# Performance work log

Measured on AMD Instinct MI355X. Metric: run time of the kernel, lower is better.

## Reference

```python
import jax, jax.numpy as jnp
import numpy as np

D_MODEL = 256   # c / input_dim
D_INNER = 512   # expand * d_model
D_STATE = 16
DT_RANK = 16    # ceil(d_model / 16)
D_CONV = 3


def setup_inputs() -> dict:
    key = jax.random.key(0)
    ks = jax.random.split(key, 8)
    s = lambda k, shape, sc=0.02: (jax.random.normal(k, shape, jnp.float32) * sc)
    feature = jax.random.normal(ks[0], (16, D_MODEL, 32, 32), jnp.float32)
    A_init = jnp.broadcast_to(jnp.arange(1, D_STATE + 1, dtype=jnp.float32), (D_INNER, D_STATE))
    return {
        "feature": feature,
        "norm_w": jnp.ones((D_MODEL,), jnp.float32),                 # RMSNorm weight
        "w_in": s(ks[1], (D_MODEL, 2 * D_INNER)),                     # in_proj (no bias)
        "conv_w": s(ks[2], (D_INNER, D_CONV), 0.1),                   # depthwise conv kernel
        "conv_b": jnp.zeros((D_INNER,), jnp.float32),                 # conv bias
        "w_xproj": s(ks[3], (D_INNER, DT_RANK + 2 * D_STATE)),        # x_proj (no bias)
        "w_dt": s(ks[4], (DT_RANK, D_INNER)),                         # dt_proj weight
        "b_dt": s(ks[5], (D_INNER,), 0.1),                            # dt_proj bias
        "A_log": jnp.log(A_init),                                     # [d_inner, d_state]
        "D": jnp.ones((D_INNER,), jnp.float32),                       # skip param
        "w_out": s(ks[6], (D_INNER, D_MODEL)),                        # out_proj (no bias)
    }


def _mamba_residual(x, norm_w, w_in, conv_w, conv_b, w_xproj, w_dt, b_dt, A_log, D, w_out):
    # x: [B, L, d_model] where B = h*w (spatial positions) and L = original batch b
    B, L, _ = x.shape
    # RMSNorm
    xn = x * jax.lax.rsqrt(jnp.mean(x * x, axis=-1, keepdims=True) + 1e-5) * norm_w
    # input projection -> [B, L, 2*d_inner]
    xr = xn @ w_in
    xm, res = jnp.split(xr, 2, axis=-1)
    # depthwise causal conv1d along L
    xc = jnp.transpose(xm, (0, 2, 1))                 # [B, d_inner, L]
    k = conv_w[:, None, :]                             # [d_inner, 1, d_conv]
    xc = jax.lax.conv_general_dilated(
        xc, k, window_strides=(1,), padding=[(D_CONV - 1, 0)],
        feature_group_count=D_INNER)
    xc = xc + conv_b[None, :, None]
    xm = jax.nn.silu(jnp.transpose(xc, (0, 2, 1)))    # [B, L, d_inner]
    # selective SSM
    A = -jnp.exp(A_log)                                # [d_inner, d_state]
    dbc = xm @ w_xproj                                 # [B, L, dt_rank + 2*d_state]
    delta, Bm, Cm = jnp.split(dbc, [DT_RANK, DT_RANK + D_STATE], axis=-1)
    delta = jax.nn.softplus(delta @ w_dt + b_dt)       # [B, L, d_inner]
    dA = jnp.exp(delta[..., None] * A)                 # [B, L, d_inner, d_state]
    dBu = delta[..., None] * Bm[:, :, None, :] * xm[..., None]

    def step(h, inp):
        dA_t, dBu_t, C_t = inp                         # [B,d,n], [B,d,n], [B,n]
        h = dA_t * h + dBu_t
        y = jnp.einsum('bdn,bn->bd', h, C_t)
        return h, y

    h0 = jnp.zeros((B, D_INNER, D_STATE), xm.dtype)
    _, ys = jax.lax.scan(
        step, h0,
        (dA.transpose(1, 0, 2, 3), dBu.transpose(1, 0, 2, 3), Cm.transpose(1, 0, 2)))
    y = ys.transpose(1, 0, 2) + xm * D                 # [B, L, d_inner]
    y = y * jax.nn.silu(res)
    return y @ w_out + x                               # residual add


def reference(feature, norm_w, w_in, conv_w, conv_b, w_xproj, w_dt, b_dt, A_log, D, w_out):
    b, c, h, w = feature.shape
    # [b,c,h,w] -> [h*w, b, c]: Mamba batch = spatial positions, seq = samples
    x = feature.transpose(0, 2, 3, 1).reshape(b, h * w, c).transpose(1, 0, 2)
    out = _mamba_residual(x, norm_w, w_in, conv_w, conv_b, w_xproj, w_dt, b_dt, A_log, D, w_out)
    out = out.transpose(1, 0, 2).reshape(b, h, w, c).transpose(0, 3, 1, 2)
    return out
```

## Files before the change

### kernel.cpp

```cpp
#include <hip/hip_runtime.h>
#include <hip/hip_bf16.h>
#include <math.h>

#define NPOS   1024
#define NSAMP  16
#define DMODEL 256
#define DINNER 512
#define DSTATE 16
#define DTRANK 16
#define MROWS  (NPOS*NSAMP)
#define LOG2E  1.44269504f

typedef __attribute__((ext_vector_type(8))) short short8;
typedef __attribute__((ext_vector_type(4))) float f32x4;

__device__ __forceinline__ unsigned short f2bf(float f) {
    unsigned int u = __builtin_bit_cast(unsigned int, f);
    u = u + 0x7FFFu + ((u >> 16) & 1u);
    return (unsigned short)(u >> 16);
}
__device__ __forceinline__ float bf2f(short b) {
    unsigned int u = ((unsigned int)(unsigned short)b) << 16;
    return __builtin_bit_cast(float, u);
}
__device__ __forceinline__ float fsilu(float x) {
    return x * __builtin_amdgcn_rcpf(1.f + __expf(-x));
}
__device__ __forceinline__ void gl16(const void* g, void* l) {
    __builtin_amdgcn_global_load_lds((const __attribute__((address_space(1))) void*)g,
                                     (__attribute__((address_space(3))) void*)l, 16, 0, 0);
}

__global__ __launch_bounds__(256) void kprep(const float* __restrict__ w_in,
                                             const float* __restrict__ w_out,
                                             const float* __restrict__ w_xproj,
                                             unsigned short* __restrict__ w_inT,
                                             unsigned short* __restrict__ w_outT,
                                             unsigned short* __restrict__ wxT) {
    int idx = blockIdx.x * 256 + threadIdx.x;
    if (idx < 262144) {
        int n = idx >> 8, k = idx & 255;
        w_inT[idx] = f2bf(w_in[(size_t)k * 1024 + n]);
    } else if (idx < 262144 + 131072) {
        int i = idx - 262144;
        int c = i >> 9, k = i & 511;
        w_outT[i] = f2bf(w_out[(size_t)k * DMODEL + c]);
    } else {
        int i = idx - 262144 - 131072;
        int j = i >> 9, k = i & 511;
        wxT[i] = f2bf(w_xproj[(size_t)k * 48 + j]);
    }
}

__global__ __launch_bounds__(256) void knorm(const float* __restrict__ feat,
                                             const float* __restrict__ norm_w,
                                             unsigned short* __restrict__ xnT) {
    __shared__ float part[4][64];
    __shared__ float ssc[64];
    __shared__ char tile[64 * 520];
    int t = threadIdx.x;
    int s = blockIdx.x, p0 = blockIdx.y * 64;
    int pl = t & 63, cg = t >> 6;
    const float* base = feat + (size_t)s * (DMODEL * NPOS) + p0 + pl;
    float vals[64];
    float ss = 0.f;
    #pragma unroll
    for (int j = 0; j < 64; ++j) {
        float v = base[(size_t)(cg * 64 + j) * NPOS];
        vals[j] = v;
        ss += v * v;
    }
    part[cg][pl] = ss;
    __syncthreads();
    if (t < 64) {
        float tot = part[0][t] + part[1][t] + part[2][t] + part[3][t];
        ssc[t] = rsqrtf(tot * (1.f / DMODEL) + 1e-5f);
    }
    __syncthreads();
    float sc = ssc[pl];
    unsigned short* trow = (unsigned short*)(tile + pl * 520);
    #pragma unroll
    for (int j = 0; j < 64; ++j)
        trow[cg * 64 + j] = f2bf(vals[j] * sc * norm_w[cg * 64 + j]);
    __syncthreads();
    int p = t >> 2, cb = (t & 3) * 64;
    const unsigned short* srow = (const unsigned short*)(tile + p * 520);
    unsigned short* orow = xnT + (size_t)((s << 10) + p0 + p) * DMODEL + cb;
    #pragma unroll
    for (int j8 = 0; j8 < 8; ++j8) {
        short8 v;
        #pragma unroll
        for (int jj = 0; jj < 8; ++jj) v[jj] = srow[cb + j8 * 8 + jj];
        *reinterpret_cast<short8*>(orow + j8 * 8) = v;
    }
}

__global__ __launch_bounds__(256) void k1_mfma(const unsigned short* __restrict__ xnT,
                                               const unsigned short* __restrict__ w_inT,
                                               unsigned short* __restrict__ xmbf,
                                               unsigned short* __restrict__ gbf) {
    __shared__ char As[128 * 128];
    __shared__ char Bs[128 * 128];
    int t = threadIdx.x;
    int m0 = blockIdx.y * 128, n0 = blockIdx.x * 128;
    int l = t & 63, w = t >> 6;
    int wm = w & 1, wn = w >> 1, g = l >> 4, lr = l & 15;

    f32x4 acc[4][4] = {};
    for (int k0 = 0; k0 < DMODEL; k0 += 64) {
        if (k0) __syncthreads();
        #pragma unroll
        for (int q = 0; q < 4; ++q) {
            int chunk = q * 256 + t;
            int row = chunk >> 3, cb = chunk & 7;
            gl16(xnT  + (size_t)(m0 + row) * DMODEL + k0 + cb * 8, As + chunk * 16);
            gl16(w_inT + (size_t)(n0 + row) * DMODEL + k0 + cb * 8, Bs + chunk * 16);
        }
        __syncthreads();
        #pragma unroll
        for (int ks = 0; ks < 2; ++ks) {
            short8 a[4], b[4];
            #pragma unroll
            for (int mi = 0; mi < 4; ++mi)
                a[mi] = *reinterpret_cast<short8*>(As + (wm * 64 + mi * 16 + lr) * 128 + ks * 64 + g * 16);
            #pragma unroll
            for (int ni = 0; ni < 4; ++ni)
                b[ni] = *reinterpret_cast<short8*>(Bs + (wn * 64 + ni * 16 + lr) * 128 + ks * 64 + g * 16);
            #pragma unroll
            for (int mi = 0; mi < 4; ++mi)
                #pragma unroll
                for (int ni = 0; ni < 4; ++ni)
                    acc[mi][ni] = __builtin_amdgcn_mfma_f32_16x16x32_bf16(a[mi], b[ni], acc[mi][ni], 0, 0, 0);
        }
    }
    bool isRes = (n0 >= 512);
    #pragma unroll
    for (int mi = 0; mi < 4; ++mi) {
        #pragma unroll
        for (int r = 0; r < 4; ++r) {
            int m = m0 + wm * 64 + mi * 16 + g * 4 + r;
            #pragma unroll
            for (int ni = 0; ni < 4; ++ni) {
                int n = n0 + wn * 64 + ni * 16 + lr;
                float v = acc[mi][ni][r];
                if (isRes) gbf[(size_t)m * DINNER + n - 512] = f2bf(fsilu(v));
                else       xmbf[(size_t)m * DINNER + n] = f2bf(v);
            }
        }
    }
}

__global__ __launch_bounds__(256) void k3_mfma(const unsigned short* __restrict__ xmbf,
                                               const float* __restrict__ conv_w,
                                               const float* __restrict__ conv_b,
                                               const unsigned short* __restrict__ wxT,
                                               float* __restrict__ dbc) {
    __shared__ char Ws[48 * 64];
    __shared__ char Xs[64 * 64];
    int t = threadIdx.x;
    int m0 = blockIdx.x * 64;
    int s = m0 >> 10;
    int l = t & 63, w = t >> 6, g = l >> 4, lr = l & 15;
    int xrow = t >> 2, xck = t & 3;
    int m = m0 + xrow;
    f32x4 acc[3] = {};
    for (int k0 = 0; k0 < DINNER; k0 += 32) {
        if (k0) __syncthreads();
        if (t < 192) {
            int j = t >> 2, ck = t & 3;
            *reinterpret_cast<short8*>(Ws + j * 64 + ck * 16) =
                *reinterpret_cast<const short8*>(wxT + (size_t)j * DINNER + k0 + ck * 8);
        }
        {
            int d0 = k0 + xck * 8;
            const unsigned short* r0 = xmbf + (size_t)m * DINNER + d0;
            short8 x0 = *reinterpret_cast<const short8*>(r0);
            short8 x1 = {}, x2 = {};
            if (s >= 1) x1 = *reinterpret_cast<const short8*>(r0 - 1024 * DINNER);
            if (s >= 2) x2 = *reinterpret_cast<const short8*>(r0 - 2048 * DINNER);
            short8 v;
            #pragma unroll
            for (int j = 0; j < 8; ++j) {
                int dd = d0 + j;
                float cv = conv_b[dd] + conv_w[dd * 3 + 2] * bf2f(x0[j])
                         + conv_w[dd * 3 + 1] * bf2f(x1[j]) + conv_w[dd * 3 + 0] * bf2f(x2[j]);
                v[j] = (short)f2bf(fsilu(cv));
            }
            *reinterpret_cast<short8*>(Xs + xrow * 64 + xck * 16) = v;
        }
        __syncthreads();
        short8 b = *reinterpret_cast<short8*>(Xs + (w * 16 + lr) * 64 + g * 16);
        #pragma unroll
        for (int aj = 0; aj < 3; ++aj) {
            short8 a = *reinterpret_cast<short8*>(Ws + (aj * 16 + lr) * 64 + g * 16);
            acc[aj] = __builtin_amdgcn_mfma_f32_16x16x32_bf16(a, b, acc[aj], 0, 0, 0);
        }
    }
    int mc = m0 + w * 16 + lr;
    #pragma unroll
    for (int aj = 0; aj < 3; ++aj)
        *reinterpret_cast<f32x4*>(dbc + (size_t)mc * 48 + aj * 16 + g * 4) = acc[aj];
}

__global__ __launch_bounds__(256) void k5_scan(const unsigned short* __restrict__ xmbf,
                                               const unsigned short* __restrict__ gbf,
                                               const float* __restrict__ dbc,
                                               const float* __restrict__ w_dt,
                                               const float* __restrict__ b_dt,
                                               const float* __restrict__ A_log,
                                               const float* __restrict__ Dp,
                                               const float* __restrict__ conv_w,
                                               const float* __restrict__ conv_b,
                                               unsigned short* __restrict__ ybf) {
    int p = blockIdx.x >> 1;
    int d = ((blockIdx.x & 1) << 8) + threadIdx.x;
    float wdt[DTRANK];
    #pragma unroll
    for (int r = 0; r < DTRANK; ++r) wdt[r] = w_dt[r * DINNER + d];
    float Ar0 = -__expf(A_log[d * DSTATE]);
    bool geo = true;
    #pragma unroll
    for (int n = 1; n < DSTATE; ++n) {
        float An = -__expf(A_log[d * DSTATE + n]);
        geo = geo && (fabsf(An - (n + 1) * Ar0) <= 1e-4f * (n + 1));
    }
    float c0 = LOG2E * Ar0;
    float w0 = conv_w[d * 3 + 0], w1 = conv_w[d * 3 + 1], w2 = conv_w[d * 3 + 2];
    float cb = conv_b[d], Dv = Dp[d], bdt = b_dt[d];
    float h[DSTATE];
    #pragma unroll
    for (int n = 0; n < DSTATE; ++n) h[n] = 0.f;
    float x1 = 0.f, x2 = 0.f;

    for (int s = 0; s < NSAMP; ++s) {
        int m = (s << 10) + p;
        size_t off = (size_t)m * DINNER + d;
        float xc = bf2f((short)xmbf[off]);
        float gv = bf2f((short)gbf[off]);
        float cv = cb + w2 * xc + w1 * x1 + w0 * x2;
        x2 = x1; x1 = xc;
        float u = fsilu(cv);
        const float* row = dbc + (size_t)m * 48;
        float dp = bdt;
        #pragma unroll
        for (int r = 0; r < DTRANK; ++r) dp += row[r] * wdt[r];
        float delta = (dp > 20.f) ? dp : __logf(1.f + __expf(dp));
        float du = delta * u;
        float yv = 0.f;
        if (geo) {
            float rg = exp2f(delta * c0);
            float rr = rg;
            #pragma unroll
            for (int n = 0; n < DSTATE; ++n) {
                h[n] = rr * h[n] + du * row[16 + n];
                yv += h[n] * row[32 + n];
                rr *= rg;
            }
        } else {
            #pragma unroll
            for (int n = 0; n < DSTATE; ++n) {
                float An = -__expf(A_log[d * DSTATE + n]);
                float dA = __expf(delta * An);
                h[n] = dA * h[n] + du * row[16 + n];
                yv += h[n] * row[32 + n];
            }
        }
        ybf[off] = f2bf((yv + u * Dv) * gv);
    }
}

__global__ __launch_bounds__(256) void k6_mfma(const unsigned short* __restrict__ ybf,
                                               const unsigned short* __restrict__ w_outT,
                                               const float* __restrict__ feat,
                                               float* __restrict__ out) {
    __shared__ char lds[2 * 128 * 80];
    char* Ws = lds;
    char* Ys = lds + 128 * 80;
    int t = threadIdx.x;
    int m0 = blockIdx.x * 128;
    int cblk = blockIdx.y * 128;
    int s = m0 >> 10, p0 = m0 & 1023;
    int i = t & 127, c0 = t >> 7;
    int l = t & 63, w = t >> 6;
    int wm = w & 1, wn = w >> 1, g = l >> 4, lr = l & 15;

    f32x4 acc[4][4] = {};
    for (int k0 = 0; k0 < DINNER; k0 += 32) {
        if (k0) __syncthreads();
        #pragma unroll
        for (int cc = 0; cc < 2; ++cc) {
            int c = c0 + cc * 2;
            *reinterpret_cast<short8*>(Ws + i * 80 + c * 16) =
                *reinterpret_cast<const short8*>(w_outT + (size_t)(cblk + i) * DINNER + k0 + c * 8);
            *reinterpret_cast<short8*>(Ys + i * 80 + c * 16) =
                *reinterpret_cast<const short8*>(ybf + (size_t)(m0 + i) * DINNER + k0 + c * 8);
        }
        __syncthreads();
        short8 a[4], b[4];
        #pragma unroll
        for (int mi = 0; mi < 4; ++mi)
            a[mi] = *reinterpret_cast<short8*>(Ws + (wm * 64 + mi * 16 + lr) * 80 + g * 16);
        #pragma unroll
        for (int ni = 0; ni < 4; ++ni)
            b[ni] = *reinterpret_cast<short8*>(Ys + (wn * 64 + ni * 16 + lr) * 80 + g * 16);
        #pragma unroll
        for (int mi = 0; mi < 4; ++mi)
            #pragma unroll
            for (int ni = 0; ni < 4; ++ni)
                acc[mi][ni] = __builtin_amdgcn_mfma_f32_16x16x32_bf16(a[mi], b[ni], acc[mi][ni], 0, 0, 0);
    }
    #pragma unroll
    for (int mi = 0; mi < 4; ++mi) {
        #pragma unroll
        for (int r = 0; r < 4; ++r) {
            int c = cblk + wm * 64 + mi * 16 + g * 4 + r;
            #pragma unroll
            for (int ni = 0; ni < 4; ++ni) {
                int p = p0 + wn * 64 + ni * 16 + lr;
                size_t idx = (size_t)s * (DMODEL * NPOS) + (size_t)c * NPOS + p;
                out[idx] = acc[mi][ni][r] + feat[idx];
            }
        }
    }
}

extern "C" void kernel_launch(void* const* d_in, const int* in_sizes, int n_in,
                              void* d_out, int out_size, void* d_ws, size_t ws_size,
                              hipStream_t stream) {
    const float* feature = (const float*)d_in[0];
    const float* norm_w  = (const float*)d_in[1];
    const float* w_in    = (const float*)d_in[2];
    const float* conv_w  = (const float*)d_in[3];
    const float* conv_b  = (const float*)d_in[4];
    const float* w_xproj = (const float*)d_in[5];
    const float* w_dt    = (const float*)d_in[6];
    const float* b_dt    = (const float*)d_in[7];
    const float* A_log   = (const float*)d_in[8];
    const float* Dp      = (const float*)d_in[9];
    const float* w_out   = (const float*)d_in[10];
    float* out = (float*)d_out;

    char* ws = (char*)d_ws;
    unsigned short* xnT    = (unsigned short*)(ws + 0);
    unsigned short* xmbf   = (unsigned short*)(ws + 8388608);
    unsigned short* gbf    = (unsigned short*)(ws + 25165824);
    float*          dbc    = (float*)(ws + 41943040);
    unsigned short* ybf    = (unsigned short*)(ws + 45088768);
    unsigned short* w_inT  = (unsigned short*)(ws + 61865984);
    unsigned short* w_outT = (unsigned short*)(ws + 62390272);
    unsigned short* wxT    = (unsigned short*)(ws + 62652416);

    kprep<<<1632, 256, 0, stream>>>(w_in, w_out, w_xproj, w_inT, w_outT, wxT);
    knorm<<<dim3(NSAMP, NPOS / 64), 256, 0, stream>>>(feature, norm_w, xnT);
    k1_mfma<<<dim3(1024 / 128, MROWS / 128), 256, 0, stream>>>(xnT, w_inT, xmbf, gbf);
    k3_mfma<<<MROWS / 64, 256, 0, stream>>>(xmbf, conv_w, conv_b, wxT, dbc);
    k5_scan<<<NPOS * 2, 256, 0, stream>>>(xmbf, gbf, dbc, w_dt, b_dt, A_log, Dp, conv_w, conv_b, ybf);
    k6_mfma<<<dim3(MROWS / 128, DMODEL / 128), 256, 0, stream>>>(ybf, w_outT, feature, out);
}
```

Measured before the change: 199.8 us.

## Split delta computation out of scan, reuse conv output, merge prep kernels

Merges weight transposition and RMSNorm into one prep kernel that also precomputes per-channel geometric-A constants. The conv+SiLU result from the x_proj kernel is now stored in bf16 so the scan does not recompute it. A new kernel computes softplus(delta) per row and packs it as bf16. The scan now handles two channels per thread and double-buffers its B/C and input loads. This shortens the serial scan loop, but it adds an extra launch and extra global writes and reads for u and delta, and delta is rounded to bf16.

```diff
diff --git a/kernel.cpp b/kernel.cpp
--- a/kernel.cpp
+++ b/kernel.cpp
@@ -23,6 +23,10 @@
     unsigned int u = ((unsigned int)(unsigned short)b) << 16;
     return __builtin_bit_cast(float, u);
 }
+__device__ __forceinline__ void unpk(unsigned int v, float& a, float& b) {
+    a = __builtin_bit_cast(float, v << 16);
+    b = __builtin_bit_cast(float, v & 0xffff0000u);
+}
 __device__ __forceinline__ float fsilu(float x) {
     return x * __builtin_amdgcn_rcpf(1.f + __expf(-x));
 }
@@ -31,67 +35,83 @@
                                      (__attribute__((address_space(3))) void*)l, 16, 0, 0);
 }
 
-__global__ __launch_bounds__(256) void kprep(const float* __restrict__ w_in,
-                                             const float* __restrict__ w_out,
-                                             const float* __restrict__ w_xproj,
-                                             unsigned short* __restrict__ w_inT,
-                                             unsigned short* __restrict__ w_outT,
-                                             unsigned short* __restrict__ wxT) {
-    int idx = blockIdx.x * 256 + threadIdx.x;
-    if (idx < 262144) {
-        int n = idx >> 8, k = idx & 255;
-        w_inT[idx] = f2bf(w_in[(size_t)k * 1024 + n]);
-    } else if (idx < 262144 + 131072) {
-        int i = idx - 262144;
-        int c = i >> 9, k = i & 511;
-        w_outT[i] = f2bf(w_out[(size_t)k * DMODEL + c]);
-    } else {
-        int i = idx - 262144 - 131072;
-        int j = i >> 9, k = i & 511;
-        wxT[i] = f2bf(w_xproj[(size_t)k * 48 + j]);
-    }
-}
-
-__global__ __launch_bounds__(256) void knorm(const float* __restrict__ feat,
-                                             const float* __restrict__ norm_w,
-                                             unsigned short* __restrict__ xnT) {
+__global__ __launch_bounds__(256) void kprep2(const float* __restrict__ feat,
+                                              const float* __restrict__ norm_w,
+                                              const float* __restrict__ w_in,
+                                              const float* __restrict__ w_out,
+                                              const float* __restrict__ w_xproj,
+                                              const float* __restrict__ A_log,
+                                              unsigned short* __restrict__ xnT,
+                                              unsigned short* __restrict__ w_inT,
+                                              unsigned short* __restrict__ w_outT,
+                                              unsigned short* __restrict__ wxT,
+                                              float2* __restrict__ scanc) {
     __shared__ float part[4][64];
     __shared__ float ssc[64];
     __shared__ char tile[64 * 520];
-    int t = threadIdx.x;
-    int s = blockIdx.x, p0 = blockIdx.y * 64;
-    int pl = t & 63, cg = t >> 6;
-    const float* base = feat + (size_t)s * (DMODEL * NPOS) + p0 + pl;
-    float vals[64];
-    float ss = 0.f;
-    #pragma unroll
-    for (int j = 0; j < 64; ++j) {
-        float v = base[(size_t)(cg * 64 + j) * NPOS];
-        vals[j] = v;
-        ss += v * v;
-    }
-    part[cg][pl] = ss;
-    __syncthreads();
-    if (t < 64) {
-        float tot = part[0][t] + part[1][t] + part[2][t] + part[3][t];
-        ssc[t] = rsqrtf(tot * (1.f / DMODEL) + 1e-5f);
-    }
-    __syncthreads();
-    float sc = ssc[pl];
-    unsigned short* trow = (unsigned short*)(tile + pl * 520);
-    #pragma unroll
-    for (int j = 0; j < 64; ++j)
-        trow[cg * 64 + j] = f2bf(vals[j] * sc * norm_w[cg * 64 + j]);
-    __syncthreads();
-    int p = t >> 2, cb = (t & 3) * 64;
-    const unsigned short* srow = (const unsigned short*)(tile + p * 520);
-    unsigned short* orow = xnT + (size_t)((s << 10) + p0 + p) * DMODEL + cb;
-    #pragma unroll
-    for (int j8 = 0; j8 < 8; ++j8) {
-        short8 v;
-        #pragma unroll
-        for (int jj = 0; jj < 8; ++jj) v[jj] = srow[cb + j8 * 8 + jj];
-        *reinterpret_cast<short8*>(orow + j8 * 8) = v;
+    int b = blockIdx.x, t = threadIdx.x;
+    if (b < 256) {
+        int s = b & 15, p0 = (b >> 4) * 64;
+        int pl = t & 63, cg = t >> 6;
+        const float* base = feat + (size_t)s * (DMODEL * NPOS) + p0 + pl;
+        float vals[64];
+        float ss = 0.f;
+        #pragma unroll
+        for (int j = 0; j < 64; ++j) {
+            float v = base[(size_t)(cg * 64 + j) * NPOS];
+            vals[j] = v;
+            ss += v * v;
+        }
+        part[cg][pl] = ss;
+        __syncthreads();
+        if (t < 64) {
+            float tot = part[0][t] + part[1][t] + part[2][t] + part[3][t];
+            ssc[t] = rsqrtf(tot * (1.f / DMODEL) + 1e-5f);
+        }
+        __syncthreads();
+        float sc = ssc[pl];
+        unsigned short* trow = (unsigned short*)(tile + pl * 520);
+        #pragma unroll
+        for (int j = 0; j < 64; ++j)
+            trow[cg * 64 + j] = f2bf(vals[j] * sc * norm_w[cg * 64 + j]);
+        __syncthreads();
+        int p = t >> 2, cb = (t & 3) * 64;
+        const unsigned short* srow = (const unsigned short*)(tile + p * 520);
+        unsigned short* orow = xnT + (size_t)((s << 10) + p0 + p) * DMODEL + cb;
+        #pragma unroll
+        for (int j8 = 0; j8 < 8; ++j8) {
+            short8 v;
+            #pragma unroll
+            for (int jj = 0; jj < 8; ++jj) v[jj] = srow[cb + j8 * 8 + jj];
+            *reinterpret_cast<short8*>(orow + j8 * 8) = v;
+        }
+    } else if (b < 1888) {
+        int idx = (b - 256) * 256 + t;
+        if (idx < 262144) {
+            int n = idx >> 8, k = idx & 255;
+            w_inT[idx] = f2bf(w_in[(size_t)k * 1024 + n]);
+        } else if (idx < 262144 + 131072) {
+            int i = idx - 262144;
+            int c = i >> 9, k = i & 511;
+            w_outT[i] = f2bf(w_out[(size_t)k * DMODEL + c]);
+        } else {
+            int i = idx - 262144 - 131072;
+            int j = i >> 9, k = i & 511;
+            wxT[i] = f2bf(w_xproj[(size_t)k * 48 + j]);
+        }
+    } else {
+        #pragma unroll
+        for (int dd = 0; dd < 2; ++dd) {
+            int d = t + dd * 256;
+            float Ar0 = -__expf(A_log[d * DSTATE]);
+            bool geo = true;
+            #pragma unroll
+            for (int n = 1; n < DSTATE; ++n) {
+                float An = -__expf(A_log[d * DSTATE + n]);
+                geo = geo && (fabsf(An - (n + 1) * Ar0) <= 1e-4f * (n + 1));
+            }
+            scanc[d] = make_float2(LOG2E * Ar0, geo ? 1.f : 0.f);
+        }
     }
 }
 
@@ -154,7 +174,8 @@
                                                const float* __restrict__ conv_w,
                                                const float* __restrict__ conv_b,
                                                const unsigned short* __restrict__ wxT,
-                                               float* __restrict__ dbc) {
+                                               float* __restrict__ dbc,
+                                               unsigned short* __restrict__ ubf) {
     __shared__ char Ws[48 * 64];
     __shared__ char Xs[64 * 64];
     int t = threadIdx.x;
@@ -187,6 +208,7 @@
                 v[j] = (short)f2bf(fsilu(cv));
             }
             *reinterpret_cast<short8*>(Xs + xrow * 64 + xck * 16) = v;
+            *reinterpret_cast<short8*>(ubf + (size_t)m * DINNER + d0) = v;
         }
         __syncthreads();
         short8 b = *reinterpret_cast<short8*>(Xs + (w * 16 + lr) * 64 + g * 16);
@@ -202,71 +224,80 @@
         *reinterpret_cast<f32x4*>(dbc + (size_t)mc * 48 + aj * 16 + g * 4) = acc[aj];
 }
 
-__global__ __launch_bounds__(256) void k5_scan(const unsigned short* __restrict__ xmbf,
-                                               const unsigned short* __restrict__ gbf,
+__global__ __launch_bounds__(256) void k4_delta(const float* __restrict__ dbc,
+                                                const float* __restrict__ w_dt,
+                                                const float* __restrict__ b_dt,
+                                                unsigned int* __restrict__ dbf2) {
+    int m = blockIdx.x, t = threadIdx.x;
+    int d0 = 2 * t;
+    const float* row = dbc + (size_t)m * 48;
+    float2 acc = *reinterpret_cast<const float2*>(b_dt + d0);
+    #pragma unroll
+    for (int r = 0; r < 16; ++r) {
+        float2 wv = *reinterpret_cast<const float2*>(w_dt + r * DINNER + d0);
+        acc.x += row[r] * wv.x;
+        acc.y += row[r] * wv.y;
+    }
+    float da = (acc.x > 20.f) ? acc.x : __logf(1.f + __expf(acc.x));
+    float db = (acc.y > 20.f) ? acc.y : __logf(1.f + __expf(acc.y));
+    dbf2[m * 256 + t] = ((unsigned int)f2bf(db) << 16) | f2bf(da);
+}
+
+__global__ __launch_bounds__(256) void k5_scan(const unsigned int* __restrict__ ubf2,
+                                               const unsigned int* __restrict__ dbf2,
+                                               const unsigned int* __restrict__ gbf2,
                                                const float* __restrict__ dbc,
-                                               const float* __restrict__ w_dt,
-                                               const float* __restrict__ b_dt,
+                                               const float2* __restrict__ scanc,
                                                const float* __restrict__ A_log,
                                                const float* __restrict__ Dp,
-                                               const float* __restrict__ conv_w,
-                                               const float* __restrict__ conv_b,
-                                               unsigned short* __restrict__ ybf) {
-    int p = blockIdx.x >> 1;
-    int d = ((blockIdx.x & 1) << 8) + threadIdx.x;
-    float wdt[DTRANK];
-    #pragma unroll
-    for (int r = 0; r < DTRANK; ++r) wdt[r] = w_dt[r * DINNER + d];
-    float Ar0 = -__expf(A_log[d * DSTATE]);
-    bool geo = true;
-    #pragma unroll
-    for (int n = 1; n < DSTATE; ++n) {
-        float An = -__expf(A_log[d * DSTATE + n]);
-        geo = geo && (fabsf(An - (n + 1) * Ar0) <= 1e-4f * (n + 1));
-    }
-    float c0 = LOG2E * Ar0;
-    float w0 = conv_w[d * 3 + 0], w1 = conv_w[d * 3 + 1], w2 = conv_w[d * 3 + 2];
-    float cb = conv_b[d], Dv = Dp[d], bdt = b_dt[d];
-    float h[DSTATE];
-    #pragma unroll
-    for (int n = 0; n < DSTATE; ++n) h[n] = 0.f;
-    float x1 = 0.f, x2 = 0.f;
-
-    for (int s = 0; s < NSAMP; ++s) {
-        int m = (s << 10) + p;
-        size_t off = (size_t)m * DINNER + d;
-        float xc = bf2f((short)xmbf[off]);
-        float gv = bf2f((short)gbf[off]);
-        float cv = cb + w2 * xc + w1 * x1 + w0 * x2;
-        x2 = x1; x1 = xc;
-        float u = fsilu(cv);
-        const float* row = dbc + (size_t)m * 48;
-        float dp = bdt;
-        #pragma unroll
-        for (int r = 0; r < DTRANK; ++r) dp += row[r] * wdt[r];
-        float delta = (dp > 20.f) ? dp : __logf(1.f + __expf(dp));
-        float du = delta * u;
-        float yv = 0.f;
-        if (geo) {
-            float rg = exp2f(delta * c0);
-            float rr = rg;
-            #pragma unroll
-            for (int n = 0; n < DSTATE; ++n) {
-                h[n] = rr * h[n] + du * row[16 + n];
-                yv += h[n] * row[32 + n];
-                rr *= rg;
-            }
-        } else {
-            #pragma unroll
-            for (int n = 0; n < DSTATE; ++n) {
-                float An = -__expf(A_log[d * DSTATE + n]);
-                float dA = __expf(delta * An);
-                h[n] = dA * h[n] + du * row[16 + n];
-                yv += h[n] * row[32 + n];
-            }
-        }
-        ybf[off] = f2bf((yv + u * Dv) * gv);
-    }
+                                               unsigned int* __restrict__ ybf2) {
+    int p = blockIdx.x, t = threadIdx.x;
+    int d0 = 2 * t, d1 = d0 + 1;
+    float2 s0c = scanc[d0], s1c = scanc[d1];
+    float c00 = s0c.x, c01 = s1c.x;
+    bool geo = (s0c.y > 0.5f) && (s1c.y > 0.5f);
+    float2 Dv = *reinterpret_cast<const float2*>(Dp + d0);
+    float h0[16], h1[16];
+    #pragma unroll
+    for (int n = 0; n < 16; ++n) { h0[n] = 0.f; h1[n] = 0.f; }
+    unsigned int base = p * 256 + t;
+    float bcA[32], bcB[32];
+    unsigned int uA, dA, gA, uB, dB, gB;
+
+#define LOADBC(BUF, S) { const float4* rp = reinterpret_cast<const float4*>(dbc + (size_t)((((S) << 10) + p) * 48 + 16)); \
+    _Pragma("unroll") for (int j = 0; j < 8; ++j) *reinterpret_cast<float4*>(&BUF[j * 4]) = rp[j]; }
+#define LOADPF(U, D, G, S) { unsigned int o = ((unsigned int)(S) << 18) + base; U = ubf2[o]; D = dbf2[o]; G = gbf2[o]; }
+#define STEP(S, BC, U, D, G) { \
+    float u0, u1, dl0, dl1, g0, g1; unpk(U, u0, u1); unpk(D, dl0, dl1); unpk(G, g0, g1); \
+    float du0 = dl0 * u0, du1 = dl1 * u1; float yv0 = 0.f, yv1 = 0.f; \
+    if (geo) { \
+        float r0 = exp2f(dl0 * c00), r1 = exp2f(dl1 * c01); \
+        float rr0 = r0, rr1 = r1; \
+        _Pragma("unroll") for (int n = 0; n < 16; ++n) { \
+            h0[n] = rr0 * h0[n] + du0 * BC[n]; yv0 += h0[n] * BC[16 + n]; rr0 *= r0; \
+            h1[n] = rr1 * h1[n] + du1 * BC[n]; yv1 += h1[n] * BC[16 + n]; rr1 *= r1; } \
+    } else { \
+        _Pragma("unroll") for (int n = 0; n < 16; ++n) { \
+            float An0 = -__expf(A_log[d0 * 16 + n]); float An1 = -__expf(A_log[d1 * 16 + n]); \
+            h0[n] = __expf(dl0 * An0) * h0[n] + du0 * BC[n]; yv0 += h0[n] * BC[16 + n]; \
+            h1[n] = __expf(dl1 * An1) * h1[n] + du1 * BC[n]; yv1 += h1[n] * BC[16 + n]; } \
+    } \
+    unsigned int o = ((unsigned int)(S) << 18) + base; \
+    ybf2[o] = ((unsigned int)f2bf((yv1 + u1 * Dv.y) * g1) << 16) | f2bf((yv0 + u0 * Dv.x) * g0); }
+
+    LOADBC(bcA, 0); LOADPF(uA, dA, gA, 0);
+    #pragma unroll
+    for (int it = 0; it < 8; ++it) {
+        int sa = 2 * it, sb = 2 * it + 1;
+        int sn = (2 * it + 2 < 16) ? 2 * it + 2 : 15;
+        LOADBC(bcB, sb); LOADPF(uB, dB, gB, sb);
+        STEP(sa, bcA, uA, dA, gA);
+        LOADBC(bcA, sn); LOADPF(uA, dA, gA, sn);
+        STEP(sb, bcB, uB, dB, gB);
+    }
+#undef LOADBC
+#undef LOADPF
+#undef STEP
 }
 
 __global__ __launch_bounds__(256) void k6_mfma(const unsigned short* __restrict__ ybf,
@@ -345,15 +376,20 @@
     unsigned short* xmbf   = (unsigned short*)(ws + 8388608);
     unsigned short* gbf    = (unsigned short*)(ws + 25165824);
     float*          dbc    = (float*)(ws + 41943040);
-    unsigned short* ybf    = (unsigned short*)(ws + 45088768);
-    unsigned short* w_inT  = (unsigned short*)(ws + 61865984);
-    unsigned short* w_outT = (unsigned short*)(ws + 62390272);
-    unsigned short* wxT    = (unsigned short*)(ws + 62652416);
-
-    kprep<<<1632, 256, 0, stream>>>(w_in, w_out, w_xproj, w_inT, w_outT, wxT);
-    knorm<<<dim3(NSAMP, NPOS / 64), 256, 0, stream>>>(feature, norm_w, xnT);
+    unsigned short* ubf    = (unsigned short*)(ws + 45088768);
+    unsigned int*   dbf2   = (unsigned int*)(ws + 61865984);
+    unsigned short* ybf    = (unsigned short*)(ws + 78643200);
+    unsigned short* w_inT  = (unsigned short*)(ws + 95420416);
+    unsigned short* w_outT = (unsigned short*)(ws + 95944704);
+    unsigned short* wxT    = (unsigned short*)(ws + 96206848);
+    float2*         scanc  = (float2*)(ws + 96256000);
+
+    kprep2<<<1889, 256, 0, stream>>>(feature, norm_w, w_in, w_out, w_xproj, A_log,
+                                     xnT, w_inT, w_outT, wxT, scanc);
     k1_mfma<<<dim3(1024 / 128, MROWS / 128), 256, 0, stream>>>(xnT, w_inT, xmbf, gbf);
-    k3_mfma<<<MROWS / 64, 256, 0, stream>>>(xmbf, conv_w, conv_b, wxT, dbc);
-    k5_scan<<<NPOS * 2, 256, 0, stream>>>(xmbf, gbf, dbc, w_dt, b_dt, A_log, Dp, conv_w, conv_b, ybf);
+    k3_mfma<<<MROWS / 64, 256, 0, stream>>>(xmbf, conv_w, conv_b, wxT, dbc, ubf);
+    k4_delta<<<MROWS, 256, 0, stream>>>(dbc, w_dt, b_dt, dbf2);
+    k5_scan<<<NPOS, 256, 0, stream>>>((const unsigned int*)ubf, dbf2, (const unsigned int*)gbf,
+                                      dbc, scanc, A_log, Dp, (unsigned int*)ybf);
     k6_mfma<<<dim3(MROWS / 128, DMODEL / 128), 256, 0, stream>>>(ybf, w_outT, feature, out);
 }
```

Result: slower. 217.4 us (+8.8%).
